# Optimization experiments

Measured on AMD Instinct MI355X. Metric: run time of the kernel, lower is better.

The kernel has to match this reference:

```python
import jax, jax.numpy as jnp
import numpy as np

NUM_HEADS = 8
NVIEW = 5
EPS = 1e-6


def setup_inputs() -> dict:
    key = jax.random.key(0)
    k1, k2, k3 = jax.random.split(key, 3)
    BV, HW, C = 20, 4096, 256
    x = jax.random.normal(k1, (BV, HW, C), dtype=jnp.float32)
    # torch.nn.Linear default init ~ U(-1/sqrt(in), 1/sqrt(in)); scale randn similarly
    W_qkv = jax.random.normal(k2, (C, 3 * C), dtype=jnp.float32) * (1.0 / np.sqrt(C))
    W_proj = jax.random.normal(k3, (C, C), dtype=jnp.float32) * (1.0 / np.sqrt(C))
    b_proj = jnp.zeros((C,), dtype=jnp.float32)
    return {"x": x, "W_qkv": W_qkv, "W_proj": W_proj, "b_proj": b_proj}


def reference(x, W_qkv, W_proj, b_proj):
    BV, HW, C = x.shape
    V = NVIEW
    B = BV // V
    H = NUM_HEADS
    d = C // H
    L = V * HW

    # merge views into one long sequence per batch element
    xb = x.reshape(B, L, C)

    # qkv projection (qkv_bias=False) -> [B, L, 3, H, d]
    qkv = (xb @ W_qkv).reshape(B, L, 3, H, d)
    q = qkv[:, :, 0]  # [B, L, H, d]
    k = qkv[:, :, 1]
    v = qkv[:, :, 2]

    # elu + 1 feature map, computed in float32 (as in the autocast-disabled block)
    q = (jax.nn.elu(q) + 1.0).astype(jnp.float32)
    k = (jax.nn.elu(k) + 1.0).astype(jnp.float32)
    v = v.astype(jnp.float32)

    # linear attention: kv = sum_l k_l (x) v_l  -> [B, H, m, d]
    kv = jnp.einsum('nlhd,nlhm->nhmd', k, v)
    # normalizer z = 1 / (q . sum_l k_l)  -> [B, L, H]
    k_sum = k.sum(axis=1)  # [B, H, d]
    z = 1.0 / (jnp.einsum('nlhd,nhd->nlh', q, k_sum) + EPS)
    # output y -> [B, L, H, m]
    y = jnp.einsum('nlhd,nhmd,nlh->nlhm', q, kv, z)

    y = y.reshape(BV, HW, C)
    return y @ W_proj + b_proj
```

## Files before the change

### kernel.cpp

```cpp
#include <hip/hip_runtime.h>

#define M_ROWS 81920
#define KDIM 256
#define NQKV 768
#define LROWS 20480
#define EPSV 1e-6f
#define KV_CHUNKS 160

using bf16x8 = __attribute__((ext_vector_type(8))) short;
using f32x4  = __attribute__((ext_vector_type(4))) float;

static __device__ __forceinline__ unsigned short f2bf(float f) {
  union { float f; unsigned int u; } c; c.f = f;
  unsigned int u = c.u;
  u += 0x7fff + ((u >> 16) & 1);
  return (unsigned short)(u >> 16);
}
static __device__ __forceinline__ float bf2f(unsigned short h) {
  union { unsigned int u; float f; } c; c.u = ((unsigned int)h) << 16;
  return c.f;
}

static __device__ __forceinline__ void async_cp16(const void* g, void* l) {
  __builtin_amdgcn_global_load_lds(
      (const __attribute__((address_space(1))) void*)(unsigned long long)g,
      (__attribute__((address_space(3))) void*)(unsigned int)(unsigned long long)l,
      16, 0, 0);
}

__global__ void cvt_x(const float* __restrict__ x, unsigned short* __restrict__ xb) {
  long i = ((long)blockIdx.x * blockDim.x + threadIdx.x) * 4;
  float4 v = *(const float4*)(x + i);
  ushort4 o;
  o.x = f2bf(v.x); o.y = f2bf(v.y); o.z = f2bf(v.z); o.w = f2bf(v.w);
  *(ushort4*)(xb + i) = o;
}

__global__ __launch_bounds__(256)
void transpose_w(const float* __restrict__ w, unsigned short* __restrict__ wt) {
  __shared__ unsigned short lds[64][258];
  int n0 = blockIdx.x * 64;
  int t = threadIdx.x;
#pragma unroll 4
  for (int it = 0; it < 64; it++) {
    int k = (t >> 6) + 4 * it;
    int n = t & 63;
    lds[n][k] = f2bf(w[(size_t)k * NQKV + n0 + n]);
  }
  __syncthreads();
#pragma unroll
  for (int it = 0; it < 16; it++) {
    int idx = it * 256 + t;
    int n = idx >> 6, c4 = (idx & 63) * 4;
    ushort4 v;
    v.x = lds[n][c4]; v.y = lds[n][c4 + 1]; v.z = lds[n][c4 + 2]; v.w = lds[n][c4 + 3];
    *(ushort4*)(wt + (size_t)(n0 + n) * 256 + c4) = v;
  }
}

template <int EPI>
__global__ __launch_bounds__(256, 3)
void gemm_bt(const unsigned short* __restrict__ A,
             const unsigned short* __restrict__ Bt,
             void* __restrict__ C,
             const float* __restrict__ bias) {
  __shared__ unsigned short As[128 * 32];
  __shared__ unsigned short Bs[128 * 32];
  const int K = 256;
  const int N = (EPI == 0) ? NQKV : 256;
  const int NT = (EPI == 0) ? 6 : 2;
  int t = threadIdx.x;
  int lane = t & 63;
  int w = t >> 6;

  int id = blockIdx.x;
  int xcd = id & 7;
  int local = id >> 3;
  int mt = local / NT;
  int nt = local - mt * NT;
  int mtile = xcd * 80 + mt;
  int m0 = mtile * 128;
  int n0 = nt * 128;
  const unsigned short* Bp = Bt;
  if (EPI == 1) Bp += (size_t)(mtile / 160) * 256 * 256;

  f32x4 acc[4][4];
#pragma unroll
  for (int i = 0; i < 4; i++)
#pragma unroll
    for (int j = 0; j < 4; j++) acc[i][j] = (f32x4){0.f, 0.f, 0.f, 0.f};

  int wm = w & 1, wn = w >> 1;
  int fm_s = lane & 15;
  int p_s = lane >> 4;

  for (int kt = 0; kt < 8; kt++) {
    int k0 = kt * 32;
    __syncthreads();
#pragma unroll
    for (int q = 0; q < 2; q++) {
      int g = w * 2 + q;
      int row = g * 16 + fm_s;
      async_cp16(A + (size_t)(m0 + row) * K + k0 + p_s * 8, As + (size_t)(g * 64 + lane) * 8);
      async_cp16(Bp + (size_t)(n0 + row) * K + k0 + p_s * 8, Bs + (size_t)(g * 64 + lane) * 8);
    }
    __syncthreads();
    bf16x8 af[4], bfr[4];
#pragma unroll
    for (int i = 0; i < 4; i++)
      af[i] = *(const bf16x8*)(As + (size_t)((i + 4 * wm) * 64 + lane) * 8);
#pragma unroll
    for (int j = 0; j < 4; j++)
      bfr[j] = *(const bf16x8*)(Bs + (size_t)((j + 4 * wn) * 64 + lane) * 8);
#pragma unroll
    for (int i = 0; i < 4; i++)
#pragma unroll
      for (int j = 0; j < 4; j++)
        acc[i][j] = __builtin_amdgcn_mfma_f32_16x16x32_bf16(af[i], bfr[j], acc[i][j], 0, 0, 0);
  }

  int quad = lane >> 4;
  int col = lane & 15;
#pragma unroll
  for (int i = 0; i < 4; i++) {
#pragma unroll
    for (int j = 0; j < 4; j++) {
      int gm_base = m0 + wm * 64 + i * 16 + quad * 4;
      int gn = n0 + wn * 64 + j * 16 + col;
#pragma unroll
      for (int r = 0; r < 4; r++) {
        float v = acc[i][j][r];
        int gm = gm_base + r;
        if (EPI == 0) {
          if (gn < 512) v = (v > 0.f) ? v + 1.f : __expf(v);
          ((unsigned short*)C)[(size_t)gm * N + gn] = f2bf(v);
        } else {
          ((float*)C)[(size_t)gm * N + gn] = v + bias[gn];
        }
      }
    }
  }
}

__global__ __launch_bounds__(512)
void kv_reduce(const unsigned short* __restrict__ qkv, float* __restrict__ kvp) {
  __shared__ unsigned short s[32 * 512];
  int chunk = blockIdx.x;
  int n = blockIdx.y;
  int t = threadIdx.x;
  int lane = t & 63;
  int w = t >> 6;
  long r0 = (long)n * LROWS + (long)chunk * 128;

  float acc[4][4] = {};
  float ks[4] = {};
  int mg = lane >> 3;
  int m0 = mg * 4, d0 = (lane & 7) * 4;

  for (int tile = 0; tile < 4; tile++) {
    __syncthreads();
#pragma unroll
    for (int q = 0; q < 4; q++) {
      int c = t + q * 512;
      int row = c >> 6, part = c & 63;
      async_cp16(qkv + (size_t)(r0 + tile * 32 + row) * 768 + 256 + part * 8,
                 s + (size_t)c * 8);
    }
    __syncthreads();
#pragma unroll 4
    for (int row = 0; row < 32; row++) {
      ushort4 kk = *(const ushort4*)(s + row * 512 + w * 32 + d0);
      ushort4 vv = *(const ushort4*)(s + row * 512 + 256 + w * 32 + m0);
      float kf[4] = {bf2f(kk.x), bf2f(kk.y), bf2f(kk.z), bf2f(kk.w)};
      float vf[4] = {bf2f(vv.x), bf2f(vv.y), bf2f(vv.z), bf2f(vv.w)};
#pragma unroll
      for (int i = 0; i < 4; i++)
#pragma unroll
        for (int j = 0; j < 4; j++) acc[i][j] += vf[i] * kf[j];
      if (mg == 0) {
        ks[0] += kf[0]; ks[1] += kf[1]; ks[2] += kf[2]; ks[3] += kf[3];
      }
    }
  }
  float* o = kvp + ((size_t)(n * KV_CHUNKS + chunk) * 8 + w) * 1056;
#pragma unroll
  for (int i = 0; i < 4; i++)
#pragma unroll
    for (int j = 0; j < 4; j++) o[(m0 + i) * 32 + d0 + j] = acc[i][j];
  if (mg == 0) {
#pragma unroll
    for (int j = 0; j < 4; j++) o[1024 + d0 + j] = ks[j];
  }
}

__global__ __launch_bounds__(256)
void kv_combine1(const float* __restrict__ kvp, float* __restrict__ kvp2) {
  int b = blockIdx.x;
  int pair = b >> 3, o = b & 7;
  int n = pair >> 3, h = pair & 7;
  int t = threadIdx.x;
  float a0 = 0.f, a1 = 0.f, a2 = 0.f, a3 = 0.f, a4 = 0.f;
  const float* base = kvp + ((size_t)(n * KV_CHUNKS) * 8 + h) * 1056;
  for (int j = 0; j < KV_CHUNKS / 8; j++) {
    const float* p = base + (size_t)(o + 8 * j) * 8 * 1056;
    a0 += p[t]; a1 += p[t + 256]; a2 += p[t + 512]; a3 += p[t + 768];
    if (t < 32) a4 += p[1024 + t];
  }
  float* oo = kvp2 + (size_t)b * 1056;
  oo[t] = a0; oo[t + 256] = a1; oo[t + 512] = a2; oo[t + 768] = a3;
  if (t < 32) oo[1024 + t] = a4;
}

__global__ __launch_bounds__(256)
void kv_combine2(const float* __restrict__ kvp2, float* __restrict__ kv,
                 float* __restrict__ ksum) {
  int pair = blockIdx.x;
  int t = threadIdx.x;
  float a0 = 0.f, a1 = 0.f, a2 = 0.f, a3 = 0.f, a4 = 0.f;
  const float* base = kvp2 + (size_t)pair * 8 * 1056;
#pragma unroll
  for (int s = 0; s < 8; s++) {
    const float* p = base + (size_t)s * 1056;
    a0 += p[t]; a1 += p[t + 256]; a2 += p[t + 512]; a3 += p[t + 768];
    if (t < 32) a4 += p[1024 + t];
  }
  float* kvo = kv + (size_t)pair * 1024;
  kvo[t] = a0; kvo[t + 256] = a1; kvo[t + 512] = a2; kvo[t + 768] = a3;
  if (t < 32) ksum[pair * 32 + t] = a4;
}

__global__ __launch_bounds__(256)
void make_g(const float* __restrict__ kv, const float* __restrict__ wproj,
            unsigned short* __restrict__ gt) {
  __shared__ float kvs[1024];
  int pair = blockIdx.x;
  int n = pair >> 3, h = pair & 7;
  int c = threadIdx.x;
  for (int i = c; i < 1024; i += 256) kvs[i] = kv[(size_t)pair * 1024 + i];
  __syncthreads();
  float acc[32];
#pragma unroll
  for (int d = 0; d < 32; d++) acc[d] = 0.f;
  for (int m = 0; m < 32; m++) {
    float wp = wproj[(size_t)(h * 32 + m) * 256 + c];
#pragma unroll
    for (int d = 0; d < 32; d++) acc[d] += kvs[m * 32 + d] * wp;
  }
  unsigned short* o = gt + ((size_t)n * 256 + c) * 256 + h * 32;
#pragma unroll
  for (int d = 0; d < 32; d++) o[d] = f2bf(acc[d]);
}

__global__ __launch_bounds__(256)
void scale_q(const unsigned short* __restrict__ qkv, const float* __restrict__ ksum,
             unsigned short* __restrict__ qp) {
  int t = threadIdx.x;
  int lane32 = t & 31;
  int rsub = t >> 5;
  long r0 = (long)blockIdx.x * 64;
  for (int p = 0; p < 8; p++) {
    long r = r0 + p * 8 + rsub;
    int n = (int)(r / LROWS);
    const unsigned short* q = qkv + r * 768 + lane32 * 8;
    ushort4 a = *(const ushort4*)(q);
    ushort4 b = *(const ushort4*)(q + 4);
    float qf[8] = {bf2f(a.x), bf2f(a.y), bf2f(a.z), bf2f(a.w),
                   bf2f(b.x), bf2f(b.y), bf2f(b.z), bf2f(b.w)};
    const float* ks = ksum + n * 256 + lane32 * 8;
    float sacc = 0.f;
#pragma unroll
    for (int i = 0; i < 8; i++) sacc += qf[i] * ks[i];
    sacc += __shfl_xor(sacc, 1);
    sacc += __shfl_xor(sacc, 2);
    float z = 1.f / (sacc + EPSV);
    ushort4 oa, ob;
    oa.x = f2bf(qf[0] * z); oa.y = f2bf(qf[1] * z);
    oa.z = f2bf(qf[2] * z); oa.w = f2bf(qf[3] * z);
    ob.x = f2bf(qf[4] * z); ob.y = f2bf(qf[5] * z);
    ob.z = f2bf(qf[6] * z); ob.w = f2bf(qf[7] * z);
    unsigned short* o = qp + r * 256 + lane32 * 8;
    *(ushort4*)o = oa;
    *(ushort4*)(o + 4) = ob;
  }
}

extern "C" void kernel_launch(void* const* d_in, const int* in_sizes, int n_in,
                              void* d_out, int out_size, void* d_ws, size_t ws_size,
                              hipStream_t stream) {
  (void)in_sizes; (void)n_in; (void)out_size; (void)ws_size;
  const float* x = (const float*)d_in[0];
  const float* Wqkv = (const float*)d_in[1];
  const float* Wproj = (const float*)d_in[2];
  const float* bproj = (const float*)d_in[3];
  float* out = (float*)d_out;

  char* ws = (char*)d_ws;
  unsigned short* xbf    = (unsigned short*)(ws);
  float*          kvp    = (float*)(ws);
  float*          kvp2   = (float*)(ws + 33554432);
  unsigned short* wqkvt  = (unsigned short*)(ws + 41943040);
  unsigned short* qkv_bf = (unsigned short*)(ws + 42336256);
  float*          kv     = (float*)(ws + 168165376);
  float*          ksum   = (float*)(ws + 168296448);
  unsigned short* gt     = (unsigned short*)(ws + 168300544);
  unsigned short* qp     = (unsigned short*)(ws + 168824832);

  cvt_x<<<M_ROWS * KDIM / 1024, 256, 0, stream>>>(x, xbf);
  transpose_w<<<NQKV / 64, 256, 0, stream>>>(Wqkv, wqkvt);
  gemm_bt<0><<<3840, 256, 0, stream>>>(xbf, wqkvt, qkv_bf, nullptr);
  kv_reduce<<<dim3(KV_CHUNKS, 4), 512, 0, stream>>>(qkv_bf, kvp);
  kv_combine1<<<256, 256, 0, stream>>>(kvp, kvp2);
  kv_combine2<<<32, 256, 0, stream>>>(kvp2, kv, ksum);
  make_g<<<32, 256, 0, stream>>>(kv, Wproj, gt);
  scale_q<<<M_ROWS / 64, 256, 0, stream>>>(qkv_bf, ksum, qp);
  gemm_bt<1><<<1280, 256, 0, stream>>>(qp, gt, out, bproj);
}
```

Measured before the change: 332.0 us.

## Use XOR-swizzled LDS tiles and swap MFMA operands for vectorized epilogue stores

Global-to-LDS loads now fetch four 16-byte segments per row from consecutive threads, and their LDS slot is XOR-swizzled to avoid bank conflicts when fragments are read back. The MFMA operands are swapped so each lane holds four consecutive output columns. This lets the epilogue write packed ushort4 (bf16) or float4 stores and load the bias as a float4 instead of scattered scalar stores. The aim is better coalescing of global reads and writes. It relies on the swizzle on the write side and the read side staying consistent.

```diff
diff --git a/kernel.cpp b/kernel.cpp
--- a/kernel.cpp
+++ b/kernel.cpp
@@ -91,52 +91,62 @@
     for (int j = 0; j < 4; j++) acc[i][j] = (f32x4){0.f, 0.f, 0.f, 0.f};
 
   int wm = w & 1, wn = w >> 1;
-  int fm_s = lane & 15;
-  int p_s = lane >> 4;
+  int fm = lane & 15;
+  int fq = lane >> 4;
+  int xr = (fm >> 2) & 3;
+
+  int sr0 = t >> 2, sp = (t & 3) ^ ((t >> 4) & 3);
+  int sr1 = sr0 + 64;
 
   for (int kt = 0; kt < 8; kt++) {
     int k0 = kt * 32;
     __syncthreads();
-#pragma unroll
-    for (int q = 0; q < 2; q++) {
-      int g = w * 2 + q;
-      int row = g * 16 + fm_s;
-      async_cp16(A + (size_t)(m0 + row) * K + k0 + p_s * 8, As + (size_t)(g * 64 + lane) * 8);
-      async_cp16(Bp + (size_t)(n0 + row) * K + k0 + p_s * 8, Bs + (size_t)(g * 64 + lane) * 8);
-    }
+    async_cp16(A + (size_t)(m0 + sr0) * K + k0 + sp * 8, As + (size_t)t * 8);
+    async_cp16(A + (size_t)(m0 + sr1) * K + k0 + sp * 8, As + (size_t)(t + 256) * 8);
+    async_cp16(Bp + (size_t)(n0 + sr0) * K + k0 + sp * 8, Bs + (size_t)t * 8);
+    async_cp16(Bp + (size_t)(n0 + sr1) * K + k0 + sp * 8, Bs + (size_t)(t + 256) * 8);
     __syncthreads();
     bf16x8 af[4], bfr[4];
 #pragma unroll
+    for (int i = 0; i < 4; i++) {
+      int row = wm * 64 + i * 16 + fm;
+      af[i] = *(const bf16x8*)(As + (size_t)(row * 4 + (fq ^ xr)) * 8);
+    }
+#pragma unroll
+    for (int j = 0; j < 4; j++) {
+      int row = wn * 64 + j * 16 + fm;
+      bfr[j] = *(const bf16x8*)(Bs + (size_t)(row * 4 + (fq ^ xr)) * 8);
+    }
+#pragma unroll
     for (int i = 0; i < 4; i++)
-      af[i] = *(const bf16x8*)(As + (size_t)((i + 4 * wm) * 64 + lane) * 8);
-#pragma unroll
-    for (int j = 0; j < 4; j++)
-      bfr[j] = *(const bf16x8*)(Bs + (size_t)((j + 4 * wn) * 64 + lane) * 8);
-#pragma unroll
-    for (int i = 0; i < 4; i++)
 #pragma unroll
       for (int j = 0; j < 4; j++)
-        acc[i][j] = __builtin_amdgcn_mfma_f32_16x16x32_bf16(af[i], bfr[j], acc[i][j], 0, 0, 0);
-  }
-
-  int quad = lane >> 4;
-  int col = lane & 15;
+        acc[i][j] = __builtin_amdgcn_mfma_f32_16x16x32_bf16(bfr[j], af[i], acc[i][j], 0, 0, 0);
+  }
+
 #pragma unroll
   for (int i = 0; i < 4; i++) {
+    int gm = m0 + wm * 64 + i * 16 + fm;
 #pragma unroll
     for (int j = 0; j < 4; j++) {
-      int gm_base = m0 + wm * 64 + i * 16 + quad * 4;
-      int gn = n0 + wn * 64 + j * 16 + col;
-#pragma unroll
-      for (int r = 0; r < 4; r++) {
-        float v = acc[i][j][r];
-        int gm = gm_base + r;
-        if (EPI == 0) {
-          if (gn < 512) v = (v > 0.f) ? v + 1.f : __expf(v);
-          ((unsigned short*)C)[(size_t)gm * N + gn] = f2bf(v);
-        } else {
-          ((float*)C)[(size_t)gm * N + gn] = v + bias[gn];
+      int gnb = n0 + wn * 64 + j * 16 + fq * 4;
+      if (EPI == 0) {
+        float v0 = acc[i][j][0], v1 = acc[i][j][1], v2 = acc[i][j][2], v3 = acc[i][j][3];
+        if (gnb < 512) {
+          v0 = (v0 > 0.f) ? v0 + 1.f : __expf(v0);
+          v1 = (v1 > 0.f) ? v1 + 1.f : __expf(v1);
+          v2 = (v2 > 0.f) ? v2 + 1.f : __expf(v2);
+          v3 = (v3 > 0.f) ? v3 + 1.f : __expf(v3);
         }
+        ushort4 pk;
+        pk.x = f2bf(v0); pk.y = f2bf(v1); pk.z = f2bf(v2); pk.w = f2bf(v3);
+        *(ushort4*)((unsigned short*)C + (size_t)gm * N + gnb) = pk;
+      } else {
+        float4 bi = *(const float4*)(bias + gnb);
+        float4 o;
+        o.x = acc[i][j][0] + bi.x; o.y = acc[i][j][1] + bi.y;
+        o.z = acc[i][j][2] + bi.z; o.w = acc[i][j][3] + bi.w;
+        *(float4*)((float*)C + (size_t)gm * N + gnb) = o;
       }
     }
   }
```

Result: faster. 313.5 us (-5.6%).
